# Optimization experiments

Measured on AMD Instinct MI355X. Metric: run time of the kernel, lower is better.

## Reference

```python
import jax, jax.numpy as jnp
import numpy as np

LEAKY = 0.1
NSAMPLE = 16


def _gather_group(p, idx):
    # p: [B, N, C], idx: [B, S, K] -> [B, S, K, C]
    return jax.vmap(lambda pb, ib: pb[ib])(p, idx)


def _knn_idx(x, k):
    # x: [B, N, 3]; squared pairwise distances, smallest-k indices
    sq = jnp.sum(x * x, axis=-1)  # [B, N]
    d = sq[:, :, None] + sq[:, None, :] - 2.0 * jnp.einsum('bnc,bmc->bnm', x, x)
    _, idx = jax.lax.top_k(-d, k)  # [B, N, K]
    return idx


def setup_inputs() -> dict:
    key = jax.random.key(0)
    k1, k2, k3, k4, k5 = jax.random.split(key, 5)
    B, N, D = 4, 8192, 32
    m0, m1, m2 = 32, 32, 64
    xyz = jax.random.normal(k1, (B, 3, N), dtype=jnp.float32)
    points = jax.random.normal(k2, (B, D, N), dtype=jnp.float32)
    # Conv2d 1x1 weights (kernel dims squeezed): [out, in]
    W0 = jax.random.normal(k3, (m0, D + 3), dtype=jnp.float32) * (1.0 / np.sqrt(D + 3))
    W1 = jax.random.normal(k4, (m1, m0), dtype=jnp.float32) * (1.0 / np.sqrt(m0))
    W2 = jax.random.normal(k5, (m2, m1), dtype=jnp.float32) * (1.0 / np.sqrt(m1))
    return {'xyz': xyz, 'points': points, 'W0': W0, 'W1': W1, 'W2': W2}


def reference(xyz, points, W0, W1, W2):
    lrelu = lambda x: jax.nn.leaky_relu(x, LEAKY)
    xyz_t = jnp.swapaxes(xyz, 1, 2)  # [B, N, 3]
    # pre-transform point features with feature part of first conv weight
    feat = jnp.einsum('oc,bcn->bno', W0[:, 3:], points)  # [B, N, m0]
    idx = _knn_idx(xyz_t, NSAMPLE)  # [B, N, K]
    grouped_xyz = _gather_group(xyz_t, idx)              # [B, N, K, 3]
    grouped_norm = grouped_xyz - xyz_t[:, :, None, :]    # relative coords
    grouped_feat = _gather_group(feat, idx)              # [B, N, K, m0]
    # first conv: xyz-part applied to relative coords + already-transformed feats
    x = jnp.einsum('oc,bnkc->bonk', W0[:, :3], grouped_norm) \
        + jnp.transpose(grouped_feat, (0, 3, 1, 2))      # [B, m0, N, K]
    x = lrelu(x)
    x = lrelu(jnp.einsum('oc,bcnk->bonk', W1, x))        # [B, m1, N, K]
    x = lrelu(jnp.einsum('oc,bcnk->bonk', W2, x))        # [B, m2, N, K]
    return jnp.max(x, axis=-1)                           # [B, m2, N]
```

## Files before the change

kernel.cpp:

```cpp
#include <hip/hip_runtime.h>

#define NP   8192
#define BB   4
#define DIN  32
#define M0   32
#define M1   32
#define M2   64
#define CAP  80
#define CSTR 81
#define KWV  16
#define SEG  (NP / KWV)

typedef float f32x2 __attribute__((ext_vector_type(2)));
typedef float f32x4 __attribute__((ext_vector_type(4)));
typedef short bf16x8 __attribute__((ext_vector_type(8)));

__device__ __forceinline__ float lrelu(float x) { return fmaxf(x, 0.1f * x); }
__device__ __forceinline__ unsigned umin_(unsigned a, unsigned b) { return a < b ? a : b; }
__device__ __forceinline__ unsigned umax_(unsigned a, unsigned b) { return a > b ? a : b; }

__device__ __forceinline__ unsigned fkey(float f) {
    unsigned b = __float_as_uint(f);
    return (b & 0x80000000u) ? ~b : (b | 0x80000000u);
}
__device__ __forceinline__ float funkey(unsigned k) {
    unsigned b = (k & 0x80000000u) ? (k & 0x7fffffffu) : ~k;
    return __uint_as_float(b);
}

__device__ __forceinline__ unsigned bf16rn(float f) {
    unsigned u = __float_as_uint(f);
    unsigned r = (u >> 16) & 1u;
    return (u + 0x7fffu + r) >> 16;
}

__device__ __forceinline__ f32x2 pk_fma(f32x2 a, f32x2 b, f32x2 c) {
    f32x2 d;
    asm("v_pk_fma_f32 %0, %1, %2, %3" : "=v"(d) : "v"(a), "s"(b), "v"(c));
    return d;
}

template<int CTRL>
__device__ __forceinline__ float fmax_dpp(float v) {
    int s = __builtin_amdgcn_update_dpp(0, __float_as_int(v), CTRL, 0xf, 0xf, true);
    return fmaxf(v, __int_as_float(s));
}

__device__ __forceinline__ void split_pack2(float f0, float f1, unsigned& hp, unsigned& lp) {
    unsigned u0 = __float_as_uint(f0), u1 = __float_as_uint(f1);
    unsigned h0 = u0 & 0xffff0000u, h1 = u1 & 0xffff0000u;
    hp = (u0 >> 16) | h1;
    float r0 = f0 - __uint_as_float(h0);
    float r1 = f1 - __uint_as_float(h1);
    lp = (__float_as_uint(r0) >> 16) | (__float_as_uint(r1) & 0xffff0000u);
}

__device__ __forceinline__ void wfrag(const float* wrow, bf16x8& h, bf16x8& lo) {
    float4 a = *(const float4*)(wrow);
    float4 b = *(const float4*)(wrow + 4);
    unsigned* hv = (unsigned*)&h;
    unsigned* lv = (unsigned*)&lo;
    split_pack2(a.x, a.y, hv[0], lv[0]);
    split_pack2(a.z, a.w, hv[1], lv[1]);
    split_pack2(b.x, b.y, hv[2], lv[2]);
    split_pack2(b.z, b.w, hv[3], lv[3]);
}

__device__ __forceinline__ f32x4 mfma16(bf16x8 a, bf16x8 b, f32x4 c) {
    return __builtin_amdgcn_mfma_f32_16x16x32_bf16(a, b, c, 0, 0, 0);
}

__global__ __launch_bounds__(256) void prep_kernel(
    const float* __restrict__ xyz, const float* __restrict__ points,
    const float* __restrict__ W0, float4* __restrict__ pts4,
    float4* __restrict__ ptsS, unsigned* __restrict__ featb)
{
    const int tid  = threadIdx.x;
    const int w    = __builtin_amdgcn_readfirstlane(tid >> 6);
    const int lane = tid & 63;
    const int t    = blockIdx.x * 64 + lane;
    const int b    = t >> 13;
    const int n    = t & (NP - 1);

    if (w == 0) {
        const float* xb = xyz + (size_t)b * 3 * NP;
        float x = xb[n], y = xb[NP + n], z = xb[2 * NP + n];
        float s = x * x + y * y + z * z;
        pts4[t] = make_float4(x, y, z, s);
        ptsS[t] = make_float4(-2.f * x, -2.f * y, -2.f * z, s);
    }

    const float* pb = points + (size_t)b * DIN * NP + n;
    float p[DIN];
#pragma unroll
    for (int c = 0; c < DIN; ++c) p[c] = pb[c * NP];

    uint4 outv;
    unsigned* ov = (unsigned*)&outv;
#pragma unroll
    for (int r = 0; r < 4; ++r) {
        int oe = w * 8 + 2 * r;
        float a0 = 0.f, a1 = 0.f;
#pragma unroll
        for (int c = 0; c < DIN; ++c) {
            a0 = fmaf(W0[oe * 35 + 3 + c], p[c], a0);
            a1 = fmaf(W0[(oe + 1) * 35 + 3 + c], p[c], a1);
        }
        ov[r] = bf16rn(a0) | (bf16rn(a1) << 16);
    }
    *(uint4*)(featb + (size_t)t * 16 + w * 4) = outv;
}

__global__ __launch_bounds__(1024, 8) void knn_kernel(const float4* __restrict__ pts4,
                                                      const float4* __restrict__ ptsS,
                                                      int* __restrict__ idxout)
{
    __shared__ unsigned skey[64 * 65];
    __shared__ float    sT[64];
    __shared__ int      scnt[64];
    __shared__ float    cand_t[64 * CSTR];
    __shared__ int      cand_i[64 * CSTR];

    const int tid  = threadIdx.x;
    const int w    = __builtin_amdgcn_readfirstlane(tid >> 6);
    const int lane = tid & 63;
    const int blk  = blockIdx.x;
    const int b    = blk >> 7;
    const int n0   = (blk & 127) << 6;
    const int bn0  = b * NP;
    const float4* P  = pts4 + bn0;
    const float4* S  = ptsS + bn0;
    const float4* Pq = P + n0;

    for (int i = tid; i < 64 * 65; i += 1024) skey[i] = 0xFFFFFFFFu;
    if (tid < 64) scnt[tid] = 0;
    __syncthreads();

    const int base = w * SEG;
    f32x2 sx[4], sy[4], sz[4], sw2[4];
#pragma unroll
    for (int jp = 0; jp < 4; ++jp) {
        float4 a = S[base + (2 * jp) * 64 + lane];
        float4 c = S[base + (2 * jp + 1) * 64 + lane];
        sx[jp].x = a.x;  sx[jp].y = c.x;
        sy[jp].x = a.y;  sy[jp].y = c.y;
        sz[jp].x = a.z;  sz[jp].y = c.z;
        sw2[jp].x = a.w; sw2[jp].y = c.w;
    }

#pragma unroll 1
    for (int qc = 0; qc < 8; ++qc) {
        float4 qv[8];
#pragma unroll
        for (int i = 0; i < 8; ++i) qv[i] = Pq[qc * 8 + i];
#pragma unroll
        for (int i = 0; i < 8; ++i) {
            f32x2 qx, qy, qz;
            qx.x = qv[i].x; qx.y = qv[i].x;
            qy.x = qv[i].y; qy.y = qv[i].y;
            qz.x = qv[i].z; qz.y = qv[i].z;
            f32x2 t0 = pk_fma(sz[0], qz, sw2[0]);
            f32x2 t1 = pk_fma(sz[1], qz, sw2[1]);
            f32x2 t2 = pk_fma(sz[2], qz, sw2[2]);
            f32x2 t3 = pk_fma(sz[3], qz, sw2[3]);
            t0 = pk_fma(sy[0], qy, t0);  t1 = pk_fma(sy[1], qy, t1);
            t2 = pk_fma(sy[2], qy, t2);  t3 = pk_fma(sy[3], qy, t3);
            t0 = pk_fma(sx[0], qx, t0);  t1 = pk_fma(sx[1], qx, t1);
            t2 = pk_fma(sx[2], qx, t2);  t3 = pk_fma(sx[3], qx, t3);
            float a  = fminf(fminf(t0.x, t0.y), t1.x);
            float b2 = fminf(fminf(t1.y, t2.x), t2.y);
            float c2 = fminf(fminf(t3.x, t3.y), a);
            float mn = fminf(b2, c2);
            atomicMin(&skey[(qc * 8 + i) * 65 + lane], fkey(mn));
        }
    }
    __syncthreads();

    if (tid < 64) {
        unsigned t16[16];
#pragma unroll
        for (int i = 0; i < 16; ++i) t16[i] = 0xFFFFFFFFu;
        for (int c = 0; c < 64; ++c) {
            unsigned d = skey[tid * 65 + c];
            if (d < t16[15]) {
                t16[15] = d;
#pragma unroll
                for (int i = 15; i > 0; --i) {
                    unsigned a = t16[i - 1], cc = t16[i];
                    t16[i - 1] = umin_(a, cc);
                    t16[i]     = umax_(a, cc);
                }
            }
        }
        sT[tid] = funkey(t16[15]);
    }
    __syncthreads();

#pragma unroll 1
    for (int qc = 0; qc < 8; ++qc) {
        float4 qv[8];
#pragma unroll
        for (int i = 0; i < 8; ++i) qv[i] = Pq[qc * 8 + i];
#pragma unroll
        for (int i = 0; i < 8; ++i) {
            const int q = qc * 8 + i;
            const float T = sT[q];
            f32x2 qx, qy, qz;
            qx.x = qv[i].x; qx.y = qv[i].x;
            qy.x = qv[i].y; qy.y = qv[i].y;
            qz.x = qv[i].z; qz.y = qv[i].z;
#pragma unroll
            for (int jp = 0; jp < 4; ++jp) {
                f32x2 t = pk_fma(sz[jp], qz, sw2[jp]);
                t = pk_fma(sy[jp], qy, t);
                t = pk_fma(sx[jp], qx, t);
                if (t.x <= T) {
                    int pos = atomicAdd(&scnt[q], 1);
                    if (pos < CAP) {
                        cand_t[q * CSTR + pos] = t.x;
                        cand_i[q * CSTR + pos] = base + (2 * jp) * 64 + lane;
                    }
                }
                if (t.y <= T) {
                    int pos = atomicAdd(&scnt[q], 1);
                    if (pos < CAP) {
                        cand_t[q * CSTR + pos] = t.y;
                        cand_i[q * CSTR + pos] = base + (2 * jp + 1) * 64 + lane;
                    }
                }
            }
        }
    }
    __syncthreads();

    if (tid < 64) {
        int cnt = scnt[tid];
        int* outp = idxout + ((bn0 + n0 + tid) << 4);
        float bd[16]; int bi[16];
#pragma unroll
        for (int i = 0; i < 16; ++i) { bd[i] = 3e38f; bi[i] = 0; }
        if (cnt <= CAP) {
            for (int pos = 0; pos < cnt; ++pos) {
                float d = cand_t[tid * CSTR + pos];
                int   j = cand_i[tid * CSTR + pos];
                if ((d < bd[15]) || (d == bd[15] && j < bi[15])) {
                    bd[15] = d; bi[15] = j;
#pragma unroll
                    for (int i = 15; i > 0; --i) {
                        bool sw = (bd[i] < bd[i - 1]) || (bd[i] == bd[i - 1] && bi[i] < bi[i - 1]);
                        float td = bd[i - 1]; int tj = bi[i - 1];
                        bd[i - 1] = sw ? bd[i] : td;  bi[i - 1] = sw ? bi[i] : tj;
                        bd[i]     = sw ? td : bd[i];  bi[i]     = sw ? tj : bi[i];
                    }
                }
            }
        } else {
            float4 q4 = Pq[tid];
            for (int j = 0; j < NP; ++j) {
                float4 s = S[j];
                float d = fmaf(q4.x, s.x, fmaf(q4.y, s.y, fmaf(q4.z, s.z, s.w)));
                if ((d < bd[15]) || (d == bd[15] && j < bi[15])) {
                    bd[15] = d; bi[15] = j;
#pragma unroll
                    for (int i = 15; i > 0; --i) {
                        bool sw = (bd[i] < bd[i - 1]) || (bd[i] == bd[i - 1] && bi[i] < bi[i - 1]);
                        float td = bd[i - 1]; int tj = bi[i - 1];
                        bd[i - 1] = sw ? bd[i] : td;  bi[i - 1] = sw ? bi[i] : tj;
                        bd[i]     = sw ? td : bd[i];  bi[i]     = sw ? tj : bi[i];
                    }
                }
            }
        }
#pragma unroll
        for (int i = 0; i < 16; ++i) outp[i] = bi[i];
    }
}

__global__ __launch_bounds__(256, 3) void conv_kernel(
    const float4* __restrict__ pts4, const unsigned* __restrict__ featb,
    const int* __restrict__ idx,
    const float* __restrict__ W0, const float* __restrict__ W1, const float* __restrict__ W2,
    float* __restrict__ out)
{
    __shared__ __align__(16) unsigned short sh_hi[4 * 2560];
    __shared__ __align__(16) unsigned short sh_lo[4 * 2560];
    __shared__ float so[M2][17];

    const int tid = threadIdx.x;
    const int w   = __builtin_amdgcn_readfirstlane(tid >> 6);
    const int l   = tid & 63;
    const int g   = l >> 4;
    const int q   = l & 15;
    const int k   = tid & 15;
    const int nl  = tid >> 4;
    const int blk = blockIdx.x;
    const int b   = blk >> 9;
    const int n0  = (blk & 511) << 4;
    const int n   = n0 + nl;
    const int bn  = b * NP + n;
    const int j   = idx[(bn << 4) + k];
    const int bj  = b * NP + j;

    bf16x8 w1h[2], w1l[2], w2h[4], w2l[4];
#pragma unroll
    for (int r = 0; r < 2; ++r) wfrag(W1 + (16 * r + q) * 32 + g * 8, w1h[r], w1l[r]);
#pragma unroll
    for (int rr = 0; rr < 4; ++rr) wfrag(W2 + (16 * rr + q) * 32 + g * 8, w2h[rr], w2l[rr]);

    const float4 pc = pts4[bn];
    const float4 pj = pts4[bj];
    const float rx = pj.x - pc.x, ry = pj.y - pc.y, rz = pj.z - pc.z;

    const uint4* fj = (const uint4*)(featb + (size_t)bj * 16);

    float x0[M0];
#pragma unroll
    for (int gg = 0; gg < 4; ++gg) {
        uint4 u = fj[gg];
        const unsigned* uv = (const unsigned*)&u;
#pragma unroll
        for (int r = 0; r < 4; ++r) {
            int o = gg * 8 + 2 * r;
            float fe  = __uint_as_float(uv[r] << 16);
            float fo_ = __uint_as_float(uv[r] & 0xffff0000u);
            x0[o]     = lrelu(fmaf(W0[o * 35], rx, fmaf(W0[o * 35 + 1], ry, fmaf(W0[o * 35 + 2], rz, fe))));
            x0[o + 1] = lrelu(fmaf(W0[(o + 1) * 35], rx, fmaf(W0[(o + 1) * 35 + 1], ry, fmaf(W0[(o + 1) * 35 + 2], rz, fo_))));
        }
    }

    unsigned short* hb = sh_hi + w * 2560 + l * 40;
    unsigned short* lb = sh_lo + w * 2560 + l * 40;
#pragma unroll
    for (int ch = 0; ch < 4; ++ch) {
        uint4 hv, lv;
        unsigned* hp = (unsigned*)&hv;
        unsigned* lp = (unsigned*)&lv;
#pragma unroll
        for (int p = 0; p < 4; ++p)
            split_pack2(x0[ch * 8 + 2 * p], x0[ch * 8 + 2 * p + 1], hp[p], lp[p]);
        *(uint4*)(hb + ch * 8) = hv;
        *(uint4*)(lb + ch * 8) = lv;
    }

    const unsigned short* rbh = sh_hi + w * 2560;
    const unsigned short* rbl = sh_lo + w * 2560;
    bf16x8 b1h[4], b1l[4];
#pragma unroll
    for (int t = 0; t < 4; ++t) {
        b1h[t] = *(const bf16x8*)(rbh + (16 * t + q) * 40 + g * 8);
        b1l[t] = *(const bf16x8*)(rbl + (16 * t + q) * 40 + g * 8);
    }
    const f32x4 zz = {0.f, 0.f, 0.f, 0.f};
    f32x4 acc1[2][4];
#pragma unroll
    for (int r = 0; r < 2; ++r)
#pragma unroll
        for (int t = 0; t < 4; ++t) {
            f32x4 a = mfma16(w1l[r], b1h[t], zz);
            a = mfma16(w1h[r], b1l[t], a);
            acc1[r][t] = mfma16(w1h[r], b1h[t], a);
        }

#pragma unroll
    for (int r = 0; r < 2; ++r)
#pragma unroll
        for (int t = 0; t < 4; ++t) {
            float v0 = lrelu(acc1[r][t][0]);
            float v1 = lrelu(acc1[r][t][1]);
            float v2 = lrelu(acc1[r][t][2]);
            float v3 = lrelu(acc1[r][t][3]);
            uint2 hv, lv;
            split_pack2(v0, v1, hv.x, lv.x);
            split_pack2(v2, v3, hv.y, lv.y);
            int off = (16 * t + q) * 40 + 16 * r + 4 * g;
            *(uint2*)(sh_hi + w * 2560 + off) = hv;
            *(uint2*)(sh_lo + w * 2560 + off) = lv;
        }

    bf16x8 b2h[4], b2l[4];
#pragma unroll
    for (int t = 0; t < 4; ++t) {
        b2h[t] = *(const bf16x8*)(rbh + (16 * t + q) * 40 + g * 8);
        b2l[t] = *(const bf16x8*)(rbl + (16 * t + q) * 40 + g * 8);
    }
#pragma unroll
    for (int h = 0; h < 2; ++h) {
#pragma unroll
        for (int r2 = 0; r2 < 2; ++r2) {
            const int rr = 2 * h + r2;
#pragma unroll
            for (int t = 0; t < 4; ++t) {
                f32x4 a = mfma16(w2l[rr], b2h[t], zz);
                a = mfma16(w2h[rr], b2l[t], a);
                a = mfma16(w2h[rr], b2h[t], a);
#pragma unroll
                for (int reg = 0; reg < 4; ++reg) {
                    float v = lrelu(a[reg]);
                    v = fmax_dpp<0xB1>(v);
                    v = fmax_dpp<0x4E>(v);
                    v = fmax_dpp<0x141>(v);
                    v = fmax_dpp<0x140>(v);
                    if (q == reg) so[16 * rr + 4 * g + reg][w * 4 + t] = v;
                }
            }
        }
    }
    __syncthreads();
    {
        int o = tid >> 2;
        int col = (tid & 3) << 2;
        float4 v = make_float4(so[o][col], so[o][col + 1], so[o][col + 2], so[o][col + 3]);
        *(float4*)(out + ((size_t)(b * M2 + o)) * NP + n0 + col) = v;
    }
}

extern "C" void kernel_launch(void* const* d_in, const int* in_sizes, int n_in,
                              void* d_out, int out_size, void* d_ws, size_t ws_size,
                              hipStream_t stream)
{
    const float* xyz    = (const float*)d_in[0];
    const float* points = (const float*)d_in[1];
    const float* W0     = (const float*)d_in[2];
    const float* W1     = (const float*)d_in[3];
    const float* W2     = (const float*)d_in[4];
    float* out = (float*)d_out;

    char* ws = (char*)d_ws;
    float4*   pts4  = (float4*)ws;
    float4*   ptsS  = (float4*)(ws + 0x080000);
    unsigned* featb = (unsigned*)(ws + 0x100000);
    int*      idx   = (int*)(ws + 0x300000);

    prep_kernel<<<BB * NP / 64, 256,  0, stream>>>(xyz, points, W0, pts4, ptsS, featb);
    knn_kernel <<<BB * NP / 64, 1024, 0, stream>>>(pts4, ptsS, idx);
    conv_kernel<<<BB * NP / 16, 256,  0, stream>>>(pts4, featb, idx, W0, W1, W2, out);
}
```

Baseline: 194.9 us.

## Prefetch query chunks in kNN and cut conv kernel register pressure

In the kNN kernel, the next chunk of eight query points is loaded into registers one iteration ahead in both passes, so global load latency overlaps the distance arithmetic. In the conv kernel, weight fragments are now loaded per output row-block instead of all up front, the layer-1 accumulators are consumed immediately, and the shared staging buffers are re-laid out as [wave][kgroup][row][8]. Launch bounds rise from 3 to 4 blocks per CU. The goal is lower VGPR use for higher occupancy; the costs are repeated weight fragment reads and more live registers for the prefetch in the kNN kernel.

```diff
diff --git a/kernel.cpp b/kernel.cpp
--- a/kernel.cpp
+++ b/kernel.cpp
@@ -148,11 +148,18 @@
         sw2[jp].x = a.w; sw2[jp].y = c.w;
     }
 
+    float4 qnxt[8];
+#pragma unroll
+    for (int i = 0; i < 8; ++i) qnxt[i] = Pq[i];
 #pragma unroll 1
     for (int qc = 0; qc < 8; ++qc) {
         float4 qv[8];
 #pragma unroll
-        for (int i = 0; i < 8; ++i) qv[i] = Pq[qc * 8 + i];
+        for (int i = 0; i < 8; ++i) qv[i] = qnxt[i];
+        if (qc < 7) {
+#pragma unroll
+            for (int i = 0; i < 8; ++i) qnxt[i] = Pq[(qc + 1) * 8 + i];
+        }
 #pragma unroll
         for (int i = 0; i < 8; ++i) {
             f32x2 qx, qy, qz;
@@ -196,11 +203,17 @@
     }
     __syncthreads();
 
+#pragma unroll
+    for (int i = 0; i < 8; ++i) qnxt[i] = Pq[i];
 #pragma unroll 1
     for (int qc = 0; qc < 8; ++qc) {
         float4 qv[8];
 #pragma unroll
-        for (int i = 0; i < 8; ++i) qv[i] = Pq[qc * 8 + i];
+        for (int i = 0; i < 8; ++i) qv[i] = qnxt[i];
+        if (qc < 7) {
+#pragma unroll
+            for (int i = 0; i < 8; ++i) qnxt[i] = Pq[(qc + 1) * 8 + i];
+        }
 #pragma unroll
         for (int i = 0; i < 8; ++i) {
             const int q = qc * 8 + i;
@@ -276,14 +289,14 @@
     }
 }
 
-__global__ __launch_bounds__(256, 3) void conv_kernel(
+__global__ __launch_bounds__(256, 4) void conv_kernel(
     const float4* __restrict__ pts4, const unsigned* __restrict__ featb,
     const int* __restrict__ idx,
     const float* __restrict__ W0, const float* __restrict__ W1, const float* __restrict__ W2,
     float* __restrict__ out)
 {
-    __shared__ __align__(16) unsigned short sh_hi[4 * 2560];
-    __shared__ __align__(16) unsigned short sh_lo[4 * 2560];
+    __shared__ __align__(16) unsigned short sh_hi[4][4][64][8];
+    __shared__ __align__(16) unsigned short sh_lo[4][4][64][8];
     __shared__ float so[M2][17];
 
     const int tid = threadIdx.x;
@@ -301,107 +314,85 @@
     const int j   = idx[(bn << 4) + k];
     const int bj  = b * NP + j;
 
-    bf16x8 w1h[2], w1l[2], w2h[4], w2l[4];
-#pragma unroll
-    for (int r = 0; r < 2; ++r) wfrag(W1 + (16 * r + q) * 32 + g * 8, w1h[r], w1l[r]);
-#pragma unroll
-    for (int rr = 0; rr < 4; ++rr) wfrag(W2 + (16 * rr + q) * 32 + g * 8, w2h[rr], w2l[rr]);
-
     const float4 pc = pts4[bn];
     const float4 pj = pts4[bj];
     const float rx = pj.x - pc.x, ry = pj.y - pc.y, rz = pj.z - pc.z;
 
     const uint4* fj = (const uint4*)(featb + (size_t)bj * 16);
 
-    float x0[M0];
 #pragma unroll
     for (int gg = 0; gg < 4; ++gg) {
         uint4 u = fj[gg];
         const unsigned* uv = (const unsigned*)&u;
+        uint4 hv, lv;
+        unsigned* hp = (unsigned*)&hv;
+        unsigned* lp = (unsigned*)&lv;
 #pragma unroll
         for (int r = 0; r < 4; ++r) {
             int o = gg * 8 + 2 * r;
             float fe  = __uint_as_float(uv[r] << 16);
             float fo_ = __uint_as_float(uv[r] & 0xffff0000u);
-            x0[o]     = lrelu(fmaf(W0[o * 35], rx, fmaf(W0[o * 35 + 1], ry, fmaf(W0[o * 35 + 2], rz, fe))));
-            x0[o + 1] = lrelu(fmaf(W0[(o + 1) * 35], rx, fmaf(W0[(o + 1) * 35 + 1], ry, fmaf(W0[(o + 1) * 35 + 2], rz, fo_))));
-        }
-    }
-
-    unsigned short* hb = sh_hi + w * 2560 + l * 40;
-    unsigned short* lb = sh_lo + w * 2560 + l * 40;
-#pragma unroll
-    for (int ch = 0; ch < 4; ++ch) {
-        uint4 hv, lv;
-        unsigned* hp = (unsigned*)&hv;
-        unsigned* lp = (unsigned*)&lv;
-#pragma unroll
-        for (int p = 0; p < 4; ++p)
-            split_pack2(x0[ch * 8 + 2 * p], x0[ch * 8 + 2 * p + 1], hp[p], lp[p]);
-        *(uint4*)(hb + ch * 8) = hv;
-        *(uint4*)(lb + ch * 8) = lv;
-    }
-
-    const unsigned short* rbh = sh_hi + w * 2560;
-    const unsigned short* rbl = sh_lo + w * 2560;
+            float e0 = lrelu(fmaf(W0[o * 35], rx, fmaf(W0[o * 35 + 1], ry, fmaf(W0[o * 35 + 2], rz, fe))));
+            float e1 = lrelu(fmaf(W0[(o + 1) * 35], rx, fmaf(W0[(o + 1) * 35 + 1], ry, fmaf(W0[(o + 1) * 35 + 2], rz, fo_))));
+            split_pack2(e0, e1, hp[r], lp[r]);
+        }
+        *(uint4*)&sh_hi[w][gg][l][0] = hv;
+        *(uint4*)&sh_lo[w][gg][l][0] = lv;
+    }
+
     bf16x8 b1h[4], b1l[4];
 #pragma unroll
     for (int t = 0; t < 4; ++t) {
-        b1h[t] = *(const bf16x8*)(rbh + (16 * t + q) * 40 + g * 8);
-        b1l[t] = *(const bf16x8*)(rbl + (16 * t + q) * 40 + g * 8);
+        b1h[t] = *(const bf16x8*)&sh_hi[w][g][16 * t + q][0];
+        b1l[t] = *(const bf16x8*)&sh_lo[w][g][16 * t + q][0];
     }
     const f32x4 zz = {0.f, 0.f, 0.f, 0.f};
-    f32x4 acc1[2][4];
-#pragma unroll
-    for (int r = 0; r < 2; ++r)
+#pragma unroll
+    for (int r = 0; r < 2; ++r) {
+        bf16x8 wh, wl;
+        wfrag(W1 + (16 * r + q) * 32 + g * 8, wh, wl);
 #pragma unroll
         for (int t = 0; t < 4; ++t) {
-            f32x4 a = mfma16(w1l[r], b1h[t], zz);
-            a = mfma16(w1h[r], b1l[t], a);
-            acc1[r][t] = mfma16(w1h[r], b1h[t], a);
-        }
-
-#pragma unroll
-    for (int r = 0; r < 2; ++r)
-#pragma unroll
-        for (int t = 0; t < 4; ++t) {
-            float v0 = lrelu(acc1[r][t][0]);
-            float v1 = lrelu(acc1[r][t][1]);
-            float v2 = lrelu(acc1[r][t][2]);
-            float v3 = lrelu(acc1[r][t][3]);
+            f32x4 a = mfma16(wl, b1h[t], zz);
+            a = mfma16(wh, b1l[t], a);
+            a = mfma16(wh, b1h[t], a);
+            float v0 = lrelu(a[0]);
+            float v1 = lrelu(a[1]);
+            float v2 = lrelu(a[2]);
+            float v3 = lrelu(a[3]);
             uint2 hv, lv;
             split_pack2(v0, v1, hv.x, lv.x);
             split_pack2(v2, v3, hv.y, lv.y);
-            int off = (16 * t + q) * 40 + 16 * r + 4 * g;
-            *(uint2*)(sh_hi + w * 2560 + off) = hv;
-            *(uint2*)(sh_lo + w * 2560 + off) = lv;
-        }
+            const int kg = 2 * r + (g >> 1);
+            const int ko = 4 * (g & 1);
+            *(uint2*)&sh_hi[w][kg][16 * t + q][ko] = hv;
+            *(uint2*)&sh_lo[w][kg][16 * t + q][ko] = lv;
+        }
+    }
 
     bf16x8 b2h[4], b2l[4];
 #pragma unroll
     for (int t = 0; t < 4; ++t) {
-        b2h[t] = *(const bf16x8*)(rbh + (16 * t + q) * 40 + g * 8);
-        b2l[t] = *(const bf16x8*)(rbl + (16 * t + q) * 40 + g * 8);
-    }
-#pragma unroll
-    for (int h = 0; h < 2; ++h) {
-#pragma unroll
-        for (int r2 = 0; r2 < 2; ++r2) {
-            const int rr = 2 * h + r2;
-#pragma unroll
-            for (int t = 0; t < 4; ++t) {
-                f32x4 a = mfma16(w2l[rr], b2h[t], zz);
-                a = mfma16(w2h[rr], b2l[t], a);
-                a = mfma16(w2h[rr], b2h[t], a);
-#pragma unroll
-                for (int reg = 0; reg < 4; ++reg) {
-                    float v = lrelu(a[reg]);
-                    v = fmax_dpp<0xB1>(v);
-                    v = fmax_dpp<0x4E>(v);
-                    v = fmax_dpp<0x141>(v);
-                    v = fmax_dpp<0x140>(v);
-                    if (q == reg) so[16 * rr + 4 * g + reg][w * 4 + t] = v;
-                }
+        b2h[t] = *(const bf16x8*)&sh_hi[w][g][16 * t + q][0];
+        b2l[t] = *(const bf16x8*)&sh_lo[w][g][16 * t + q][0];
+    }
+#pragma unroll
+    for (int rr = 0; rr < 4; ++rr) {
+        bf16x8 wh, wl;
+        wfrag(W2 + (16 * rr + q) * 32 + g * 8, wh, wl);
+#pragma unroll
+        for (int t = 0; t < 4; ++t) {
+            f32x4 a = mfma16(wl, b2h[t], zz);
+            a = mfma16(wh, b2l[t], a);
+            a = mfma16(wh, b2h[t], a);
+#pragma unroll
+            for (int reg = 0; reg < 4; ++reg) {
+                float v = lrelu(a[reg]);
+                v = fmax_dpp<0xB1>(v);
+                v = fmax_dpp<0x4E>(v);
+                v = fmax_dpp<0x141>(v);
+                v = fmax_dpp<0x140>(v);
+                if (q == reg) so[16 * rr + 4 * g + reg][w * 4 + t] = v;
             }
         }
     }
```

New measurement: 208.5 us. +7.0%, slower.
